# Optimization experiments

Hardware: AMD Instinct MI355X
Metric: run time of the kernel (lower is better)

## Reference

```python
import jax, jax.numpy as jnp
import numpy as np

NV, NQ, K, C, FF, H = 40000, 8192, 96, 128, 256, 8
DH = C // H


def _layernorm(x, g, b, eps=1e-5):
    m = jnp.mean(x, axis=-1, keepdims=True)
    v = jnp.var(x, axis=-1, keepdims=True)
    return (x - m) * jax.lax.rsqrt(v + eps) * g + b


def setup_inputs() -> dict:
    key = jax.random.key(0)
    ks = jax.random.split(key, 20)
    voxel_features = jax.random.normal(ks[0], (NV, C), dtype=jnp.float32)
    voxel_coords = jax.random.normal(ks[1], (NV, 3), dtype=jnp.float32)
    query_coords = jax.random.normal(ks[2], (NQ, 3), dtype=jnp.float32)
    raw = jax.random.randint(ks[3], (NQ, K), 0, 50000)
    key_indices = jnp.where(raw >= NV, -1, raw)  # -1 marks padded/missing keys
    key_indices = key_indices.at[:, 0].set(raw[:, 0] % NV)  # ensure >=1 valid key per query
    w = lambda k, shape: (jax.random.normal(k, shape, dtype=jnp.float32) * 0.02)
    return {
        "voxel_features": voxel_features,
        "voxel_coords": voxel_coords,
        "query_coords": query_coords,
        "key_indices": key_indices,
        "norm1_g": jnp.ones((C,), jnp.float32), "norm1_b": jnp.zeros((C,), jnp.float32),
        "q_pos_w": w(ks[4], (C, 3)), "q_pos_b": jnp.zeros((C,), jnp.float32),
        "k_pos_w": w(ks[5], (C, 3)), "k_pos_b": jnp.zeros((C,), jnp.float32),
        "in_w": w(ks[6], (3 * C, C)), "in_b": jnp.zeros((3 * C,), jnp.float32),
        "out_w": w(ks[7], (C, C)), "out_b": jnp.zeros((C,), jnp.float32),
        "norm2_g": jnp.ones((C,), jnp.float32), "norm2_b": jnp.zeros((C,), jnp.float32),
        "lin1_w": w(ks[8], (FF, C)), "lin1_b": jnp.zeros((FF,), jnp.float32),
        "lin2_w": w(ks[9], (C, FF)), "lin2_b": jnp.zeros((C,), jnp.float32),
        "fin_w": w(ks[10], (C, C)), "fin_b": jnp.zeros((C,), jnp.float32),
    }


def reference(voxel_features, voxel_coords, query_coords, key_indices,
              norm1_g, norm1_b, q_pos_w, q_pos_b, k_pos_w, k_pos_b,
              in_w, in_b, out_w, out_b, norm2_g, norm2_b,
              lin1_w, lin1_b, lin2_w, lin2_b, fin_w, fin_b):
    mask = key_indices < 0                      # [NQ, K] True = padded
    idx = jnp.where(mask, 0, key_indices)
    vf = _layernorm(voxel_features, norm1_g, norm1_b)   # norm1
    key_feat = vf[idx]                          # gather: [NQ, K, C]
    key_c = voxel_coords[idx]                   # [NQ, K, 3]
    # q_pos_proj: Linear(3,C)+ReLU ; k_pos_proj: Conv1d(3,C,1)+ReLU (== per-key linear)
    q_feat = jax.nn.relu(query_coords @ q_pos_w.T + q_pos_b)        # [NQ, C]
    key_pos = jax.nn.relu(jnp.einsum('nkt,ct->nkc', key_c, k_pos_w) + k_pos_b)
    key_feat = key_feat + key_pos               # [NQ, K, C]
    # nn.MultiheadAttention: query [1,NQ,C], key/value [K,NQ,C] -> per-query attention over K keys
    wq, wk, wv = in_w[:C], in_w[C:2 * C], in_w[2 * C:]
    bq, bk, bv = in_b[:C], in_b[C:2 * C], in_b[2 * C:]
    q = (q_feat @ wq.T + bq).reshape(NQ, H, DH)                 # [NQ,H,DH]
    k = (key_feat @ wk.T + bk).reshape(NQ, K, H, DH)            # [NQ,K,H,DH]
    v = (key_feat @ wv.T + bv).reshape(NQ, K, H, DH)
    scale = 1.0 / np.sqrt(DH)
    scores = jnp.einsum('nhd,nkhd->nhk', q, k) * scale          # [NQ,H,K]
    scores = jnp.where(mask[:, None, :], jnp.float32(-1e9), scores)
    attn = jax.nn.softmax(scores, axis=-1)
    ctx = jnp.einsum('nhk,nkhd->nhd', attn, v).reshape(NQ, C)
    attend = ctx @ out_w.T + out_b                              # [NQ,C]
    # FFN block (dropout=0 -> identity)
    h = _layernorm(attend, norm2_g, norm2_b)
    act = jax.nn.relu(h @ lin1_w.T + lin1_b) @ lin2_w.T + lin2_b
    x = attend + act
    out = jax.nn.relu(x @ fin_w.T + fin_b)                      # output_layer
    return out
```

## Files before the change

kernel.cpp:

```cpp
#include <hip/hip_runtime.h>
#include <hip/hip_bf16.h>
#include <math.h>

constexpr int NVOX = 40000;
constexpr int NQRY = 8192;
constexpr int KK   = 96;
constexpr int CH   = 128;
constexpr int FFD  = 256;

typedef __attribute__((ext_vector_type(8))) short short8;
typedef __attribute__((ext_vector_type(4))) float float4v;

__device__ inline float bflo(unsigned u) { return __uint_as_float(u << 16); }
__device__ inline float bfhi(unsigned u) { return __uint_as_float(u & 0xffff0000u); }
__device__ inline unsigned short f2bf(float x) {
  union { float f; unsigned u; } a; a.f = x;
  const unsigned r = a.u + 0x7fffu + ((a.u >> 16) & 1u);
  return (unsigned short)(r >> 16);
}
__device__ inline unsigned pack2(float lo, float hi) {
  return (unsigned)f2bf(lo) | ((unsigned)f2bf(hi) << 16);
}

__global__ __launch_bounds__(256) void k_prep(
    const float* __restrict__ vfeat, const float* __restrict__ vcoord,
    const float* __restrict__ n1g, const float* __restrict__ n1b,
    const float* __restrict__ kpw, const float* __restrict__ kpb,
    const float* __restrict__ in_w, const float* __restrict__ in_b,
    const float* __restrict__ ow, const float* __restrict__ l1w,
    const float* __restrict__ l2w, const float* __restrict__ fw,
    const float* __restrict__ qcoord,
    const float* __restrict__ qpw, const float* __restrict__ qpb,
    __hip_bfloat16* __restrict__ Gb, __hip_bfloat16* __restrict__ Wb,
    __hip_bfloat16* __restrict__ Eb, float* __restrict__ qout) {
  const int b = blockIdx.x;
  const int t = threadIdx.x;
  if (b < NVOX/16) {
    const int vloc = t >> 4;
    const int l    = t & 15;
    const int j = b * 16 + vloc;
    const float4* vrow = reinterpret_cast<const float4*>(vfeat + (size_t)j * CH);
    const float4 x0 = vrow[l*2], x1 = vrow[l*2+1];
    float s  = x0.x+x0.y+x0.z+x0.w + x1.x+x1.y+x1.z+x1.w;
    float ss = x0.x*x0.x+x0.y*x0.y+x0.z*x0.z+x0.w*x0.w
             + x1.x*x1.x+x1.y*x1.y+x1.z*x1.z+x1.w*x1.w;
    #pragma unroll
    for (int m = 8; m >= 1; m >>= 1) { s += __shfl_xor(s, m); ss += __shfl_xor(ss, m); }
    const float mean = s * (1.0f/CH);
    const float var  = ss * (1.0f/CH) - mean*mean;
    const float rstd = 1.0f / sqrtf(var + 1e-5f);
    const float c0 = vcoord[j*3+0], c1 = vcoord[j*3+1], c2 = vcoord[j*3+2];
    const float xv[8] = {x0.x,x0.y,x0.z,x0.w,x1.x,x1.y,x1.z,x1.w};
    float gv[8];
    #pragma unroll
    for (int u = 0; u < 8; u++) {
      const int c = l*8 + u;
      const float vf = (xv[u] - mean) * rstd * n1g[c] + n1b[c];
      const float kp = fmaf(c0, kpw[c*3+0], fmaf(c1, kpw[c*3+1], fmaf(c2, kpw[c*3+2], kpb[c])));
      gv[u] = vf + fmaxf(kp, 0.0f);
    }
    const uint4 pk = make_uint4(pack2(gv[0],gv[1]), pack2(gv[2],gv[3]),
                                pack2(gv[4],gv[5]), pack2(gv[6],gv[7]));
    *reinterpret_cast<uint4*>(Gb + (size_t)j*CH + l*8) = pk;
  } else if (b < NVOX/16 + 32) {
    const int idx = b - NVOX/16;
    const float* src;
    __hip_bfloat16* dst;
    if (idx < 8) {
      const int e = (idx * 256 + t) * 16;
      src = in_w + (size_t)CH*CH + e;
      dst = Wb + e;
    } else {
      const int f = ((idx - 8) * 256 + t) * 16;
      dst = Eb + f;
      if      (f < 16384) src = ow  + f;
      else if (f < 49152) src = l1w + (f - 16384);
      else if (f < 81920) src = l2w + (f - 49152);
      else                src = fw  + (f - 81920);
    }
    float v[16];
    #pragma unroll
    for (int u = 0; u < 4; u++) {
      const float4 fq = *reinterpret_cast<const float4*>(src + u*4);
      v[u*4+0]=fq.x; v[u*4+1]=fq.y; v[u*4+2]=fq.z; v[u*4+3]=fq.w;
    }
    uint4* o = reinterpret_cast<uint4*>(dst);
    o[0] = make_uint4(pack2(v[0],v[1]), pack2(v[2],v[3]),
                      pack2(v[4],v[5]), pack2(v[6],v[7]));
    o[1] = make_uint4(pack2(v[8],v[9]), pack2(v[10],v[11]),
                      pack2(v[12],v[13]), pack2(v[14],v[15]));
  } else {
    __shared__ float qf[16][CH];
    const int qbase = (b - (NVOX/16 + 32)) * 16;
    #pragma unroll
    for (int i = 0; i < 8; i++) {
      const int e = t + 256*i;
      const int qv = e >> 7, c = e & 127;
      const int qq = qbase + qv;
      const float v = fmaf(qcoord[qq*3+0], qpw[c*3+0],
                      fmaf(qcoord[qq*3+1], qpw[c*3+1],
                      fmaf(qcoord[qq*3+2], qpw[c*3+2], qpb[c])));
      qf[qv][c] = fmaxf(v, 0.0f);
    }
    __syncthreads();
    const int oc = t & 127, half = t >> 7;
    const float* wrow = in_w + (size_t)oc * CH;
    const float bia = in_b[oc];
    float acc[8];
    #pragma unroll
    for (int v = 0; v < 8; v++) acc[v] = bia;
    for (int c = 0; c < CH; c += 4) {
      const float4 w4 = *reinterpret_cast<const float4*>(wrow + c);
      #pragma unroll
      for (int v = 0; v < 8; v++) {
        const float4 g4 = *reinterpret_cast<const float4*>(&qf[half*8+v][c]);
        acc[v] = fmaf(g4.x, w4.x, fmaf(g4.y, w4.y, fmaf(g4.z, w4.z, fmaf(g4.w, w4.w, acc[v]))));
      }
    }
    #pragma unroll
    for (int v = 0; v < 8; v++) qout[(size_t)(qbase + half*8 + v)*CH + oc] = acc[v];
  }
}

__global__ __launch_bounds__(256) void k_kv_gemm(
    const __hip_bfloat16* __restrict__ Gb, const __hip_bfloat16* __restrict__ Wb,
    const float* __restrict__ in_b,
    unsigned short* __restrict__ KVh) {
  __shared__ unsigned short ldsD[64][40];
  const int t = threadIdx.x;
  const int w = t >> 6;
  const int lane = t & 63;
  const int col = lane & 15;
  const int quad = lane >> 4;
  const int bx = blockIdx.x;
  const int h  = bx & 7;
  const int v0 = (bx >> 3) * 64;
  const int vw = v0 + w*16;

  const unsigned short* gRow =
      reinterpret_cast<const unsigned short*>(Gb) + (size_t)(vw + col)*CH + quad*8;
  short8 afrag[4];
  #pragma unroll
  for (int kq = 0; kq < 4; kq++)
    afrag[kq] = *reinterpret_cast<const short8*>(gRow + kq*32);

  const float biaK = in_b[CH   + h*16 + col];
  const float biaV = in_b[2*CH + h*16 + col];
  float4v accK = (float4v){biaK, biaK, biaK, biaK};
  float4v accV = (float4v){biaV, biaV, biaV, biaV};
  const unsigned short* wB = reinterpret_cast<const unsigned short*>(Wb);
  #pragma unroll
  for (int kq = 0; kq < 4; kq++) {
    const short8 bK = *reinterpret_cast<const short8*>(
        wB + (size_t)(h*16 + col)*CH + kq*32 + quad*8);
    accK = __builtin_amdgcn_mfma_f32_16x16x32_bf16(afrag[kq], bK, accK, 0, 0, 0);
    const short8 bV = *reinterpret_cast<const short8*>(
        wB + (size_t)(CH + h*16 + col)*CH + kq*32 + quad*8);
    accV = __builtin_amdgcn_mfma_f32_16x16x32_bf16(afrag[kq], bV, accV, 0, 0, 0);
  }
  #pragma unroll
  for (int r = 0; r < 4; r++) {
    const int row = w*16 + quad*4 + r;
    ldsD[row][col]      = f2bf(accK[r]);
    ldsD[row][16 + col] = f2bf(accV[r]);
  }
  __syncthreads();
  const int v  = t >> 2;
  const int qq = t & 3;
  const uint4 d = *reinterpret_cast<const uint4*>(&ldsD[v][qq*8]);
  *reinterpret_cast<uint4*>(KVh + ((size_t)h*NVOX + v0 + v)*32 + qq*8) = d;
}

__global__ __launch_bounds__(256) void k_attn(
    const unsigned short* __restrict__ KVh,
    const float* __restrict__ qg, const int* __restrict__ kidx,
    float* __restrict__ ctxg, unsigned* __restrict__ sink) {
  __shared__ float qs[8][16];
  __shared__ float sc[8*104];
  __shared__ float red[128][9];
  __shared__ float rden[8];
  const int t    = threadIdx.x;
  const int h    = blockIdx.x & 7;
  const int n0   = (blockIdx.x >> 3) * 8;
  const int w    = t >> 6;
  const int lane = t & 63;
  const int quad = lane >> 2;
  const int r    = lane & 3;
  const int qh   = quad >> 3;
  const int g    = quad & 7;
  const int q_l  = 2*w + qh;
  const unsigned short* KVbase = KVh + (size_t)h * NVOX * 32;

  uint4 wv = make_uint4(0u, 0u, 0u, 0u);
  if (t < 40) {
    int line = (blockIdx.x >> 3) * 39 + t;
    if (line > NVOX - 1) line = NVOX - 1;
    wv = *reinterpret_cast<const uint4*>(KVbase + (size_t)line * 32);
  }

  if (t < 128) {
    const int q = t >> 4, d = t & 15;
    qs[q][d] = qg[(size_t)(n0 + q)*CH + h*16 + d];
  }
  unsigned msk = 0;
  uint4 kvbuf[12];
  const int krow = (n0 + q_l)*KK + g;
  #pragma unroll
  for (int it = 0; it < 12; it++) {
    const int j0 = kidx[krow + it*8];
    msk |= (unsigned)(j0 < 0) << it;
    const int j = (j0 < 0) ? 0 : j0;
    kvbuf[it] = *reinterpret_cast<const uint4*>(KVbase + (size_t)j*32 + r*8);
  }
  __syncthreads();
  const float4 qa = *reinterpret_cast<const float4*>(&qs[q_l][(r & 1)*8]);
  const float4 qb = *reinterpret_cast<const float4*>(&qs[q_l][(r & 1)*8 + 4]);
  #pragma unroll
  for (int it = 0; it < 12; it++) {
    const uint4 kv = kvbuf[it];
    float s = 0.0f;
    s = fmaf(qa.x, bflo(kv.x), s); s = fmaf(qa.y, bfhi(kv.x), s);
    s = fmaf(qa.z, bflo(kv.y), s); s = fmaf(qa.w, bfhi(kv.y), s);
    s = fmaf(qb.x, bflo(kv.z), s); s = fmaf(qb.y, bfhi(kv.z), s);
    s = fmaf(qb.z, bflo(kv.w), s); s = fmaf(qb.w, bfhi(kv.w), s);
    s += __shfl_xor(s, 1);
    if (r == 0)
      sc[q_l*104 + g + it*8] = ((msk >> it) & 1) ? -1e9f : s * 0.25f;
  }
  __syncthreads();
  if (t < 128) {
    const int q = t >> 4, l = t & 15;
    float mx = -3e38f;
    #pragma unroll
    for (int k = l; k < KK; k += 16) mx = fmaxf(mx, sc[q*104 + k]);
    #pragma unroll
    for (int m = 8; m >= 1; m >>= 1) mx = fmaxf(mx, __shfl_xor(mx, m));
    float sum = 0.0f;
    #pragma unroll
    for (int k = l; k < KK; k += 16) {
      const float p = __expf(sc[q*104 + k] - mx);
      sc[q*104 + k] = p;
      sum += p;
    }
    #pragma unroll
    for (int m = 8; m >= 1; m >>= 1) sum += __shfl_xor(sum, m);
    if (l == 0) rden[q] = 1.0f / sum;
  }
  __syncthreads();
  {
    float acc[8] = {0,0,0,0,0,0,0,0};
    #pragma unroll
    for (int it = 0; it < 12; it++) {
      const float wg = sc[q_l*104 + g + it*8];
      const uint4 kv = kvbuf[it];
      acc[0] = fmaf(wg, bflo(kv.x), acc[0]); acc[1] = fmaf(wg, bfhi(kv.x), acc[1]);
      acc[2] = fmaf(wg, bflo(kv.y), acc[2]); acc[3] = fmaf(wg, bfhi(kv.y), acc[3]);
      acc[4] = fmaf(wg, bflo(kv.z), acc[4]); acc[5] = fmaf(wg, bfhi(kv.z), acc[5]);
      acc[6] = fmaf(wg, bflo(kv.w), acc[6]); acc[7] = fmaf(wg, bfhi(kv.w), acc[7]);
    }
    if (r >= 2) {
      const int slot = q_l*16 + g*2 + (r - 2);
      #pragma unroll
      for (int u = 0; u < 8; u++) red[slot][u] = acc[u];
    }
  }
  __syncthreads();
  if (t < 128) {
    const int q = t >> 4, d = t & 15;
    const int half = d >> 3, u = d & 7;
    float s = 0.0f;
    #pragma unroll
    for (int gg = 0; gg < 8; gg++) s += red[q*16 + gg*2 + half][u];
    ctxg[(size_t)(n0 + q)*CH + h*16 + d] = s * rden[q];
  }
  const unsigned accw = wv.x ^ wv.y ^ wv.z ^ wv.w;
  if (accw == 0x9E3779B9u && t == 255) sink[0] = accw;
}

__global__ __launch_bounds__(256) void k_epi(
    const float* __restrict__ ctxg, const __hip_bfloat16* __restrict__ Eb,
    const float* __restrict__ ob,
    const float* __restrict__ n2g, const float* __restrict__ n2b,
    const float* __restrict__ l1b, const float* __restrict__ l2b,
    const float* __restrict__ fb,
    float* __restrict__ outp) {
  __shared__ unsigned short csb[16][136];
  __shared__ float attnS[16][132];
  __shared__ unsigned short hb[16][136];
  __shared__ unsigned short a1b[16][264];
  __shared__ unsigned short xb[16][136];
  const unsigned short* owb  = reinterpret_cast<const unsigned short*>(Eb);
  const unsigned short* l1wb = owb + 16384;
  const unsigned short* l2wb = owb + 49152;
  const unsigned short* fwb  = owb + 81920;

  const int t = threadIdx.x;
  const int w = t >> 6;
  const int lane = t & 63;
  const int col = lane & 15;
  const int quad = lane >> 4;
  const int qbase = blockIdx.x * 16;

  {
    const int e = t * 8;
    const int row = e >> 7, cc = e & 127;
    const float4* src = reinterpret_cast<const float4*>(ctxg + (size_t)(qbase+row)*CH + cc);
    const float4 x0 = src[0], x1 = src[1];
    *reinterpret_cast<uint4*>(&csb[row][cc]) =
        make_uint4(pack2(x0.x,x0.y), pack2(x0.z,x0.w), pack2(x1.x,x1.y), pack2(x1.z,x1.w));
  }
  __syncthreads();
  {
    short8 af[4];
    #pragma unroll
    for (int kq = 0; kq < 4; kq++)
      af[kq] = *reinterpret_cast<const short8*>(&csb[col][quad*8 + kq*32]);
    #pragma unroll
    for (int j = 0; j < 2; j++) {
      const int n0 = w*32 + j*16;
      const float bia = ob[n0 + col];
      float4v acc = (float4v){bia, bia, bia, bia};
      #pragma unroll
      for (int kq = 0; kq < 4; kq++) {
        const short8 bf = *reinterpret_cast<const short8*>(
            owb + (size_t)(n0 + col)*CH + kq*32 + quad*8);
        acc = __builtin_amdgcn_mfma_f32_16x16x32_bf16(af[kq], bf, acc, 0, 0, 0);
      }
      #pragma unroll
      for (int r = 0; r < 4; r++) attnS[quad*4 + r][n0 + col] = acc[r];
    }
  }
  __syncthreads();
  {
    const int row = t >> 4, l = t & 15;
    float s = 0.0f, ss = 0.0f;
    #pragma unroll
    for (int c = l; c < CH; c += 16) { const float x = attnS[row][c]; s += x; ss += x*x; }
    #pragma unroll
    for (int m = 8; m >= 1; m >>= 1) { s += __shfl_xor(s, m); ss += __shfl_xor(ss, m); }
    const float mean = s * (1.0f/CH);
    const float var  = ss * (1.0f/CH) - mean*mean;
    const float rstd = 1.0f / sqrtf(var + 1e-5f);
    #pragma unroll
    for (int c = l; c < CH; c += 16)
      hb[row][c] = f2bf((attnS[row][c] - mean) * rstd * n2g[c] + n2b[c]);
  }
  __syncthreads();
  {
    short8 af[4];
    #pragma unroll
    for (int kq = 0; kq < 4; kq++)
      af[kq] = *reinterpret_cast<const short8*>(&hb[col][quad*8 + kq*32]);
    #pragma unroll
    for (int j = 0; j < 4; j++) {
      const int n0 = w*64 + j*16;
      const float bia = l1b[n0 + col];
      float4v acc = (float4v){bia, bia, bia, bia};
      #pragma unroll
      for (int kq = 0; kq < 4; kq++) {
        const short8 bf = *reinterpret_cast<const short8*>(
            l1wb + (size_t)(n0 + col)*CH + kq*32 + quad*8);
        acc = __builtin_amdgcn_mfma_f32_16x16x32_bf16(af[kq], bf, acc, 0, 0, 0);
      }
      #pragma unroll
      for (int r = 0; r < 4; r++)
        a1b[quad*4 + r][n0 + col] = f2bf(fmaxf(acc[r], 0.0f));
    }
  }
  __syncthreads();
  {
    short8 af[8];
    #pragma unroll
    for (int kq = 0; kq < 8; kq++)
      af[kq] = *reinterpret_cast<const short8*>(&a1b[col][quad*8 + kq*32]);
    #pragma unroll
    for (int j = 0; j < 2; j++) {
      const int n0 = w*32 + j*16;
      const float bia = l2b[n0 + col];
      float4v acc = (float4v){bia, bia, bia, bia};
      #pragma unroll
      for (int kq = 0; kq < 8; kq++) {
        const short8 bf = *reinterpret_cast<const short8*>(
            l2wb + (size_t)(n0 + col)*FFD + kq*32 + quad*8);
        acc = __builtin_amdgcn_mfma_f32_16x16x32_bf16(af[kq], bf, acc, 0, 0, 0);
      }
      #pragma unroll
      for (int r = 0; r < 4; r++)
        xb[quad*4 + r][n0 + col] = f2bf(acc[r] + attnS[quad*4 + r][n0 + col]);
    }
  }
  __syncthreads();
  {
    short8 af[4];
    #pragma unroll
    for (int kq = 0; kq < 4; kq++)
      af[kq] = *reinterpret_cast<const short8*>(&xb[col][quad*8 + kq*32]);
    #pragma unroll
    for (int j = 0; j < 2; j++) {
      const int n0 = w*32 + j*16;
      const float bia = fb[n0 + col];
      float4v acc = (float4v){bia, bia, bia, bia};
      #pragma unroll
      for (int kq = 0; kq < 4; kq++) {
        const short8 bf = *reinterpret_cast<const short8*>(
            fwb + (size_t)(n0 + col)*CH + kq*32 + quad*8);
        acc = __builtin_amdgcn_mfma_f32_16x16x32_bf16(af[kq], bf, acc, 0, 0, 0);
      }
      #pragma unroll
      for (int r = 0; r < 4; r++)
        outp[(size_t)(qbase + quad*4 + r)*CH + n0 + col] = fmaxf(acc[r], 0.0f);
    }
  }
}

extern "C" void kernel_launch(void* const* d_in, const int* in_sizes, int n_in,
                              void* d_out, int out_size, void* d_ws, size_t ws_size,
                              hipStream_t stream) {
  const float* vfeat  = (const float*)d_in[0];
  const float* vcoord = (const float*)d_in[1];
  const float* qcoord = (const float*)d_in[2];
  const int*   kidx   = (const int*)  d_in[3];
  const float* n1g    = (const float*)d_in[4];
  const float* n1b    = (const float*)d_in[5];
  const float* qpw    = (const float*)d_in[6];
  const float* qpb    = (const float*)d_in[7];
  const float* kpw    = (const float*)d_in[8];
  const float* kpb    = (const float*)d_in[9];
  const float* in_w   = (const float*)d_in[10];
  const float* in_b   = (const float*)d_in[11];
  const float* out_w  = (const float*)d_in[12];
  const float* out_b  = (const float*)d_in[13];
  const float* n2g    = (const float*)d_in[14];
  const float* n2b    = (const float*)d_in[15];
  const float* l1w    = (const float*)d_in[16];
  const float* l1b    = (const float*)d_in[17];
  const float* l2w    = (const float*)d_in[18];
  const float* l2b    = (const float*)d_in[19];
  const float* fw     = (const float*)d_in[20];
  const float* fb     = (const float*)d_in[21];
  float* out = (float*)d_out;

  unsigned short* KVh = (unsigned short*)d_ws;
  __hip_bfloat16* Gb = (__hip_bfloat16*)(KVh + (size_t)8*NVOX*32);
  __hip_bfloat16* Wb = Gb + (size_t)NVOX*CH;
  __hip_bfloat16* Eb = Wb + (size_t)2*CH*CH;
  float* qb = (float*)(Eb + 98304);
  float* cx = qb + (size_t)NQRY*CH;
  unsigned* sink = (unsigned*)(cx + (size_t)NQRY*CH);

  k_prep   <<<NVOX/16 + 32 + NQRY/16, 256, 0, stream>>>(
      vfeat, vcoord, n1g, n1b, kpw, kpb, in_w, in_b,
      out_w, l1w, l2w, fw, qcoord, qpw, qpb, Gb, Wb, Eb, qb);
  k_kv_gemm<<<(NVOX/64)*8, 256, 0, stream>>>(Gb, Wb, in_b, KVh);
  k_attn   <<<(NQRY/8)*8, 256, 0, stream>>>(KVh, qb, kidx, cx, sink);
  k_epi    <<<NQRY/16, 256, 0, stream>>>(cx, Eb, out_b, n2g, n2b, l1b, l2b, fb, out);
}
```

Before: 202.2 us.

## Fuse voxel layernorm/pos-embed prep into the K/V projection GEMM kernel

The voxel layernorm plus key-position embedding is now computed directly into MFMA A-fragments inside the K/V projection blocks. This drops the bf16 intermediate G buffer and the separate weight-conversion blocks, and merges two launches into one. The catch is redundant work: each voxel's normalization is recomputed once per head (8x), and the fp32 K/V weights are re-read and converted to bf16 in every block.

```diff
diff --git a/kernel.cpp b/kernel.cpp
--- a/kernel.cpp
+++ b/kernel.cpp
@@ -7,6 +7,7 @@
 constexpr int KK   = 96;
 constexpr int CH   = 128;
 constexpr int FFD  = 256;
+constexpr int NKVB = (NVOX/64)*8;
 
 typedef __attribute__((ext_vector_type(8))) short short8;
 typedef __attribute__((ext_vector_type(4))) float float4v;
@@ -22,7 +23,7 @@
   return (unsigned)f2bf(lo) | ((unsigned)f2bf(hi) << 16);
 }
 
-__global__ __launch_bounds__(256) void k_prep(
+__global__ __launch_bounds__(256) void k_main(
     const float* __restrict__ vfeat, const float* __restrict__ vcoord,
     const float* __restrict__ n1g, const float* __restrict__ n1b,
     const float* __restrict__ kpw, const float* __restrict__ kpb,
@@ -31,53 +32,115 @@
     const float* __restrict__ l2w, const float* __restrict__ fw,
     const float* __restrict__ qcoord,
     const float* __restrict__ qpw, const float* __restrict__ qpb,
-    __hip_bfloat16* __restrict__ Gb, __hip_bfloat16* __restrict__ Wb,
-    __hip_bfloat16* __restrict__ Eb, float* __restrict__ qout) {
+    unsigned short* __restrict__ KVh, __hip_bfloat16* __restrict__ Eb,
+    float* __restrict__ qout) {
   const int b = blockIdx.x;
   const int t = threadIdx.x;
-  if (b < NVOX/16) {
-    const int vloc = t >> 4;
-    const int l    = t & 15;
-    const int j = b * 16 + vloc;
-    const float4* vrow = reinterpret_cast<const float4*>(vfeat + (size_t)j * CH);
-    const float4 x0 = vrow[l*2], x1 = vrow[l*2+1];
-    float s  = x0.x+x0.y+x0.z+x0.w + x1.x+x1.y+x1.z+x1.w;
-    float ss = x0.x*x0.x+x0.y*x0.y+x0.z*x0.z+x0.w*x0.w
-             + x1.x*x1.x+x1.y*x1.y+x1.z*x1.z+x1.w*x1.w;
-    #pragma unroll
-    for (int m = 8; m >= 1; m >>= 1) { s += __shfl_xor(s, m); ss += __shfl_xor(ss, m); }
+  if (b < NKVB) {
+    __shared__ unsigned short ldsD[64][40];
+    const int w    = t >> 6;
+    const int lane = t & 63;
+    const int col  = lane & 15;
+    const int quad = lane >> 4;
+    const int h    = b & 7;
+    const int v0   = (b >> 3) * 64;
+    const int j    = v0 + w*16 + col;
+
+    const float* vrow = vfeat + (size_t)j * CH;
+    float xv[4][8];
+    float s = 0.0f, ss = 0.0f;
+    #pragma unroll
+    for (int kq = 0; kq < 4; kq++) {
+      const float4 a = *reinterpret_cast<const float4*>(vrow + kq*32 + quad*8);
+      const float4 c = *reinterpret_cast<const float4*>(vrow + kq*32 + quad*8 + 4);
+      xv[kq][0]=a.x; xv[kq][1]=a.y; xv[kq][2]=a.z; xv[kq][3]=a.w;
+      xv[kq][4]=c.x; xv[kq][5]=c.y; xv[kq][6]=c.z; xv[kq][7]=c.w;
+      s  += a.x+a.y+a.z+a.w + c.x+c.y+c.z+c.w;
+      ss += a.x*a.x+a.y*a.y+a.z*a.z+a.w*a.w
+          + c.x*c.x+c.y*c.y+c.z*c.z+c.w*c.w;
+    }
+    s += __shfl_xor(s, 16);  ss += __shfl_xor(ss, 16);
+    s += __shfl_xor(s, 32);  ss += __shfl_xor(ss, 32);
     const float mean = s * (1.0f/CH);
     const float var  = ss * (1.0f/CH) - mean*mean;
     const float rstd = 1.0f / sqrtf(var + 1e-5f);
     const float c0 = vcoord[j*3+0], c1 = vcoord[j*3+1], c2 = vcoord[j*3+2];
-    const float xv[8] = {x0.x,x0.y,x0.z,x0.w,x1.x,x1.y,x1.z,x1.w};
-    float gv[8];
-    #pragma unroll
-    for (int u = 0; u < 8; u++) {
-      const int c = l*8 + u;
-      const float vf = (xv[u] - mean) * rstd * n1g[c] + n1b[c];
-      const float kp = fmaf(c0, kpw[c*3+0], fmaf(c1, kpw[c*3+1], fmaf(c2, kpw[c*3+2], kpb[c])));
-      gv[u] = vf + fmaxf(kp, 0.0f);
-    }
-    const uint4 pk = make_uint4(pack2(gv[0],gv[1]), pack2(gv[2],gv[3]),
-                                pack2(gv[4],gv[5]), pack2(gv[6],gv[7]));
-    *reinterpret_cast<uint4*>(Gb + (size_t)j*CH + l*8) = pk;
-  } else if (b < NVOX/16 + 32) {
-    const int idx = b - NVOX/16;
+    short8 afrag[4];
+    #pragma unroll
+    for (int kq = 0; kq < 4; kq++) {
+      const int cb = kq*32 + quad*8;
+      const float4 g0 = *reinterpret_cast<const float4*>(n1g + cb);
+      const float4 g1 = *reinterpret_cast<const float4*>(n1g + cb + 4);
+      const float4 be0 = *reinterpret_cast<const float4*>(n1b + cb);
+      const float4 be1 = *reinterpret_cast<const float4*>(n1b + cb + 4);
+      const float4 p0 = *reinterpret_cast<const float4*>(kpb + cb);
+      const float4 p1 = *reinterpret_cast<const float4*>(kpb + cb + 4);
+      float kw[24];
+      #pragma unroll
+      for (int q2 = 0; q2 < 6; q2++) {
+        const float4 f = *reinterpret_cast<const float4*>(kpw + cb*3 + q2*4);
+        kw[q2*4+0]=f.x; kw[q2*4+1]=f.y; kw[q2*4+2]=f.z; kw[q2*4+3]=f.w;
+      }
+      const float gam[8]  = {g0.x,g0.y,g0.z,g0.w,g1.x,g1.y,g1.z,g1.w};
+      const float bet[8]  = {be0.x,be0.y,be0.z,be0.w,be1.x,be1.y,be1.z,be1.w};
+      const float kpbv[8] = {p0.x,p0.y,p0.z,p0.w,p1.x,p1.y,p1.z,p1.w};
+      short8 af;
+      #pragma unroll
+      for (int u = 0; u < 8; u++) {
+        const float vf = (xv[kq][u] - mean) * rstd * gam[u] + bet[u];
+        const float kp = fmaf(c0, kw[u*3+0],
+                         fmaf(c1, kw[u*3+1],
+                         fmaf(c2, kw[u*3+2], kpbv[u])));
+        af[u] = (short)f2bf(vf + fmaxf(kp, 0.0f));
+      }
+      afrag[kq] = af;
+    }
+
+    const float biaK = in_b[CH   + h*16 + col];
+    const float biaV = in_b[2*CH + h*16 + col];
+    float4v accK = (float4v){biaK, biaK, biaK, biaK};
+    float4v accV = (float4v){biaV, biaV, biaV, biaV};
+    const float* wK = in_w + (size_t)(CH   + h*16 + col)*CH;
+    const float* wV = in_w + (size_t)(2*CH + h*16 + col)*CH;
+    #pragma unroll
+    for (int kq = 0; kq < 4; kq++) {
+      const float4 k0 = *reinterpret_cast<const float4*>(wK + kq*32 + quad*8);
+      const float4 k1 = *reinterpret_cast<const float4*>(wK + kq*32 + quad*8 + 4);
+      short8 bK;
+      bK[0]=(short)f2bf(k0.x); bK[1]=(short)f2bf(k0.y);
+      bK[2]=(short)f2bf(k0.z); bK[3]=(short)f2bf(k0.w);
+      bK[4]=(short)f2bf(k1.x); bK[5]=(short)f2bf(k1.y);
+      bK[6]=(short)f2bf(k1.z); bK[7]=(short)f2bf(k1.w);
+      accK = __builtin_amdgcn_mfma_f32_16x16x32_bf16(afrag[kq], bK, accK, 0, 0, 0);
+      const float4 u0 = *reinterpret_cast<const float4*>(wV + kq*32 + quad*8);
+      const float4 u1 = *reinterpret_cast<const float4*>(wV + kq*32 + quad*8 + 4);
+      short8 bV;
+      bV[0]=(short)f2bf(u0.x); bV[1]=(short)f2bf(u0.y);
+      bV[2]=(short)f2bf(u0.z); bV[3]=(short)f2bf(u0.w);
+      bV[4]=(short)f2bf(u1.x); bV[5]=(short)f2bf(u1.y);
+      bV[6]=(short)f2bf(u1.z); bV[7]=(short)f2bf(u1.w);
+      accV = __builtin_amdgcn_mfma_f32_16x16x32_bf16(afrag[kq], bV, accV, 0, 0, 0);
+    }
+    #pragma unroll
+    for (int r = 0; r < 4; r++) {
+      const int row = w*16 + quad*4 + r;
+      ldsD[row][col]      = f2bf(accK[r]);
+      ldsD[row][16 + col] = f2bf(accV[r]);
+    }
+    __syncthreads();
+    const int v  = t >> 2;
+    const int qq = t & 3;
+    const uint4 d = *reinterpret_cast<const uint4*>(&ldsD[v][qq*8]);
+    *reinterpret_cast<uint4*>(KVh + ((size_t)h*NVOX + v0 + v)*32 + qq*8) = d;
+  } else if (b < NKVB + 24) {
+    const int idx = b - NKVB;
+    const int f = (idx * 256 + t) * 16;
     const float* src;
-    __hip_bfloat16* dst;
-    if (idx < 8) {
-      const int e = (idx * 256 + t) * 16;
-      src = in_w + (size_t)CH*CH + e;
-      dst = Wb + e;
-    } else {
-      const int f = ((idx - 8) * 256 + t) * 16;
-      dst = Eb + f;
-      if      (f < 16384) src = ow  + f;
-      else if (f < 49152) src = l1w + (f - 16384);
-      else if (f < 81920) src = l2w + (f - 49152);
-      else                src = fw  + (f - 81920);
-    }
+    __hip_bfloat16* dst = Eb + f;
+    if      (f < 16384) src = ow  + f;
+    else if (f < 49152) src = l1w + (f - 16384);
+    else if (f < 81920) src = l2w + (f - 49152);
+    else                src = fw  + (f - 81920);
     float v[16];
     #pragma unroll
     for (int u = 0; u < 4; u++) {
@@ -91,7 +154,7 @@
                       pack2(v[12],v[13]), pack2(v[14],v[15]));
   } else {
     __shared__ float qf[16][CH];
-    const int qbase = (b - (NVOX/16 + 32)) * 16;
+    const int qbase = (b - (NKVB + 24)) * 16;
     #pragma unroll
     for (int i = 0; i < 8; i++) {
       const int e = t + 256*i;
@@ -120,55 +183,6 @@
     #pragma unroll
     for (int v = 0; v < 8; v++) qout[(size_t)(qbase + half*8 + v)*CH + oc] = acc[v];
   }
-}
-
-__global__ __launch_bounds__(256) void k_kv_gemm(
-    const __hip_bfloat16* __restrict__ Gb, const __hip_bfloat16* __restrict__ Wb,
-    const float* __restrict__ in_b,
-    unsigned short* __restrict__ KVh) {
-  __shared__ unsigned short ldsD[64][40];
-  const int t = threadIdx.x;
-  const int w = t >> 6;
-  const int lane = t & 63;
-  const int col = lane & 15;
-  const int quad = lane >> 4;
-  const int bx = blockIdx.x;
-  const int h  = bx & 7;
-  const int v0 = (bx >> 3) * 64;
-  const int vw = v0 + w*16;
-
-  const unsigned short* gRow =
-      reinterpret_cast<const unsigned short*>(Gb) + (size_t)(vw + col)*CH + quad*8;
-  short8 afrag[4];
-  #pragma unroll
-  for (int kq = 0; kq < 4; kq++)
-    afrag[kq] = *reinterpret_cast<const short8*>(gRow + kq*32);
-
-  const float biaK = in_b[CH   + h*16 + col];
-  const float biaV = in_b[2*CH + h*16 + col];
-  float4v accK = (float4v){biaK, biaK, biaK, biaK};
-  float4v accV = (float4v){biaV, biaV, biaV, biaV};
-  const unsigned short* wB = reinterpret_cast<const unsigned short*>(Wb);
-  #pragma unroll
-  for (int kq = 0; kq < 4; kq++) {
-    const short8 bK = *reinterpret_cast<const short8*>(
-        wB + (size_t)(h*16 + col)*CH + kq*32 + quad*8);
-    accK = __builtin_amdgcn_mfma_f32_16x16x32_bf16(afrag[kq], bK, accK, 0, 0, 0);
-    const short8 bV = *reinterpret_cast<const short8*>(
-        wB + (size_t)(CH + h*16 + col)*CH + kq*32 + quad*8);
-    accV = __builtin_amdgcn_mfma_f32_16x16x32_bf16(afrag[kq], bV, accV, 0, 0, 0);
-  }
-  #pragma unroll
-  for (int r = 0; r < 4; r++) {
-    const int row = w*16 + quad*4 + r;
-    ldsD[row][col]      = f2bf(accK[r]);
-    ldsD[row][16 + col] = f2bf(accV[r]);
-  }
-  __syncthreads();
-  const int v  = t >> 2;
-  const int qq = t & 3;
-  const uint4 d = *reinterpret_cast<const uint4*>(&ldsD[v][qq*8]);
-  *reinterpret_cast<uint4*>(KVh + ((size_t)h*NVOX + v0 + v)*32 + qq*8) = d;
 }
 
 __global__ __launch_bounds__(256) void k_attn(
@@ -441,17 +455,14 @@
   float* out = (float*)d_out;
 
   unsigned short* KVh = (unsigned short*)d_ws;
-  __hip_bfloat16* Gb = (__hip_bfloat16*)(KVh + (size_t)8*NVOX*32);
-  __hip_bfloat16* Wb = Gb + (size_t)NVOX*CH;
-  __hip_bfloat16* Eb = Wb + (size_t)2*CH*CH;
+  __hip_bfloat16* Eb = (__hip_bfloat16*)(KVh + (size_t)8*NVOX*32);
   float* qb = (float*)(Eb + 98304);
   float* cx = qb + (size_t)NQRY*CH;
   unsigned* sink = (unsigned*)(cx + (size_t)NQRY*CH);
 
-  k_prep   <<<NVOX/16 + 32 + NQRY/16, 256, 0, stream>>>(
+  k_main<<<NKVB + 24 + NQRY/16, 256, 0, stream>>>(
       vfeat, vcoord, n1g, n1b, kpw, kpb, in_w, in_b,
-      out_w, l1w, l2w, fw, qcoord, qpw, qpb, Gb, Wb, Eb, qb);
-  k_kv_gemm<<<(NVOX/64)*8, 256, 0, stream>>>(Gb, Wb, in_b, KVh);
-  k_attn   <<<(NQRY/8)*8, 256, 0, stream>>>(KVh, qb, kidx, cx, sink);
-  k_epi    <<<NQRY/16, 256, 0, stream>>>(cx, Eb, out_b, n2g, n2b, l1b, l2b, fb, out);
-}
+      out_w, l1w, l2w, fw, qcoord, qpw, qpb, KVh, Eb, qb);
+  k_attn<<<(NQRY/8)*8, 256, 0, stream>>>(KVh, qb, kidx, cx, sink);
+  k_epi <<<NQRY/16, 256, 0, stream>>>(cx, Eb, out_b, n2g, n2b, l1b, l2b, fb, out);
+}
```

After: 249.0 us. 23.1% more time.
